# Kernel tuning notes

Hardware: AMD Instinct MI355X
Metric: run time of the kernel (lower is better)

The kernel has to match this reference:

```python
import jax, jax.numpy as jnp
import numpy as np

N = 100_000   # nodes
E = 1_600_000 # edges
F = 128       # feature_dim
H = 128       # hidden_dim
C = 16        # num_classes


def setup_inputs() -> dict:
    key = jax.random.key(0)
    ks = jax.random.split(key, 7)
    x = jax.random.normal(ks[0], (N, F), dtype=jnp.float32)
    edge_index = jax.random.randint(ks[1], (2, E), 0, N, dtype=jnp.int64)
    edge_attr = jax.random.uniform(ks[2], (E,), dtype=jnp.float32)
    W1 = jax.random.normal(ks[3], (F, H), dtype=jnp.float32) / np.float32(np.sqrt(F))
    b1 = jnp.zeros((H,), jnp.float32)
    W2 = jax.random.normal(ks[4], (H, C), dtype=jnp.float32) / np.float32(np.sqrt(H))
    b2 = jnp.zeros((C,), jnp.float32)
    return {"x": x, "edge_index": edge_index, "edge_attr": edge_attr,
            "W1": W1, "b1": b1, "W2": W2, "b2": b2}


def gcn_conv(x, src, dst, ew, W, b, n):
    # PyG GCNConv: add self-loops (weight 1), symmetric degree normalization,
    # linear transform, weighted scatter-sum to destinations, bias after aggregation.
    loop = jnp.arange(n, dtype=src.dtype)
    s = jnp.concatenate([src, loop])
    d = jnp.concatenate([dst, loop])
    w = jnp.concatenate([ew, jnp.ones((n,), ew.dtype)])
    deg = jax.ops.segment_sum(w, d, num_segments=n)           # [N]
    dinv = jnp.where(deg > 0, jax.lax.rsqrt(deg), 0.0)
    norm = dinv[s] * w * dinv[d]                               # [E+N]
    h = x @ W                                                  # [N, out]
    out = jax.ops.segment_sum(h[s] * norm[:, None], d, num_segments=n)
    return out + b


def reference(x, edge_index, edge_attr, W1, b1, W2, b2):
    src, dst = edge_index[0], edge_index[1]
    h = gcn_conv(x, src, dst, edge_attr, W1, b1, N)
    h = jax.nn.relu(h)
    # dropout is identity in eval mode
    h = gcn_conv(h, src, dst, edge_attr, W2, b2, N)
    return jax.nn.softmax(h, axis=1)
```

## Files before the change

### kernel.cpp

```cpp
#include <hip/hip_runtime.h>
#include <hip/hip_fp16.h>
#include <math.h>

#define SCAN_CHUNK 2048
#define NBLK 256
#define BSH 9
#define BNODES 512


typedef __attribute__((ext_vector_type(8))) _Float16 f16x8;
typedef __attribute__((ext_vector_type(16))) float f32x16;


__global__ __launch_bounds__(256) void k_prep(const float* __restrict__ W,
                                              __half* __restrict__ W1f) {
    int tid = blockIdx.x * 256 + threadIdx.x;
    if (tid < 16384) {
        int j  = tid & 7;
        int l  = (tid >> 3) & 63;
        int ks = (tid >> 9) & 7;
        int cb = tid >> 12;
        int c = cb * 32 + (l & 31);
        int k = (l >> 5) * 8 + ks * 16 + j;
        W1f[tid] = __float2half(W[(size_t)k * 128 + c]);
    }
}


__device__ __forceinline__ void gemm1_mfma(const float* __restrict__ x,
                                           const __half* __restrict__ W1f,
                                           __half* __restrict__ h1, int n,
                                           int row0, int t, char* smem) {
    __half (*xs)[136] = (__half (*)[136])smem;
#pragma unroll
    for (int it = 0; it < 4; ++it) {
        int idx = it * 256 + t;
        int r = idx >> 5, c4 = (idx & 31) * 4;
        int gr = row0 + r;
        float4 v = (gr < n) ? *(const float4*)(x + (size_t)gr * 128 + c4)
                            : make_float4(0.f, 0.f, 0.f, 0.f);
        union { __half2 h[2]; uint2 u; } pk;
        pk.h[0] = __floats2half2_rn(v.x, v.y);
        pk.h[1] = __floats2half2_rn(v.z, v.w);
        *(uint2*)&xs[r][c4] = pk.u;
    }
    __syncthreads();

    int wv = t >> 6, lane = t & 63;
    int m = lane & 31, kh = lane >> 5;
    int col0 = wv * 32;

    f16x8 a[8], b[8];
    const __half* bp = W1f + ((size_t)wv * 8 * 64 + lane) * 8;
#pragma unroll
    for (int ks = 0; ks < 8; ++ks)
        b[ks] = *(const f16x8*)(bp + (size_t)ks * 64 * 8);
#pragma unroll
    for (int ks = 0; ks < 8; ++ks)
        a[ks] = *(const f16x8*)&xs[m][kh * 8 + ks * 16];

    f32x16 acc;
#pragma unroll
    for (int r = 0; r < 16; ++r) acc[r] = 0.f;
#pragma unroll
    for (int ks = 0; ks < 8; ++ks)
        acc = __builtin_amdgcn_mfma_f32_32x32x16_f16(a[ks], b[ks], acc, 0, 0, 0);

#pragma unroll
    for (int r = 0; r < 16; ++r) {
        int row = (r & 3) + 8 * (r >> 2) + 4 * kh;
        int g = row0 + row;
        if (g < n) h1[(size_t)g * 128 + col0 + m] = __float2half(acc[r]);
    }
}

__device__ __forceinline__ long long sl_begin(int eb, int e) {
    return ((long long)eb * e / NBLK) & ~3LL;
}


__global__ __launch_bounds__(256) void kA(const int* __restrict__ dst, int e,
                                          int* __restrict__ hist, int nbuck,
                                          const float* __restrict__ x,
                                          const __half* __restrict__ W1f,
                                          __half* __restrict__ h1, int n,
                                          int nbB, int nbG, int gbase) {
    __shared__ char smem[32 * 136 * 2];
    int bid = blockIdx.x;
    long long T = nbB + nbG;
    long long g = ((long long)bid * nbG) / T;
    bool is_g = (((long long)(bid + 1) * nbG) / T) > g;
    int t = threadIdx.x;

    if (!is_g) {
        int* cnt = (int*)smem;
        int eb = bid - (int)g;
        for (int j = t; j < nbuck; j += 256) cnt[j] = 0;
        __syncthreads();
        long long e0 = sl_begin(eb, e);
        long long e1 = (eb == NBLK - 1) ? e : sl_begin(eb + 1, e);
        for (long long i = e0 + (long long)t * 4; i + 3 < e1; i += 1024) {
            int4 d4 = *(const int4*)(dst + i);
            atomicAdd(&cnt[d4.x >> BSH], 1);
            atomicAdd(&cnt[d4.y >> BSH], 1);
            atomicAdd(&cnt[d4.z >> BSH], 1);
            atomicAdd(&cnt[d4.w >> BSH], 1);
        }
        long long vend = e0 + ((e1 - e0) & ~3LL);
        for (long long i = vend + t; i < e1; i += 256)
            atomicAdd(&cnt[dst[i] >> BSH], 1);
        __syncthreads();
        for (int j = t; j < nbuck; j += 256)
            hist[(size_t)j * NBLK + eb] = cnt[j];
        return;
    }

    gemm1_mfma(x, W1f, h1, n, (gbase + (int)g) * 32, t, smem);
}


__global__ __launch_bounds__(256) void k_scanh(int* __restrict__ hist,
                                               int* __restrict__ bsum, int nh) {
    __shared__ int sh[256];
    int b = blockIdx.x, t = threadIdx.x;
    int base = b * SCAN_CHUNK + t * 8;
    int v[8];
    int s = 0;
#pragma unroll
    for (int j = 0; j < 8; ++j) {
        int i = base + j;
        v[j] = (i < nh) ? hist[i] : 0;
        s += v[j];
    }
    sh[t] = s;
    __syncthreads();
    for (int off = 1; off < 256; off <<= 1) {
        int u = (t >= off) ? sh[t - off] : 0;
        __syncthreads();
        sh[t] += u;
        __syncthreads();
    }
    int excl = (t > 0) ? sh[t - 1] : 0;
    if (t == 255) bsum[b] = sh[255];
    int run = excl;
#pragma unroll
    for (int j = 0; j < 8; ++j) {
        int i = base + j;
        if (i < nh) hist[i] = run;
        run += v[j];
    }
}

__device__ __forceinline__ void scan_bsum(const int* __restrict__ bsum, int nbS,
                                          int* boffs, int t) {
    if (t < 32) {
        int raw = (t < nbS) ? bsum[t] : 0;
        int v = raw;
        for (int off = 1; off < 32; off <<= 1) {
            int u = __shfl_up(v, off, 64);
            if (t >= off) v += u;
        }
        boffs[t] = v - raw;
    }
}


__global__ __launch_bounds__(256) void kB(const int* __restrict__ src,
                                          const int* __restrict__ dst,
                                          const float* __restrict__ ew, int e,
                                          const int* __restrict__ hist,
                                          const int* __restrict__ bsum, int nbS,
                                          int nbuck,
                                          int2* __restrict__ bucketed,
                                          const float* __restrict__ x,
                                          const __half* __restrict__ W1f,
                                          __half* __restrict__ h1, int n,
                                          int nbB, int nbG, int gbase) {
    __shared__ char smem[32 * 136 * 2];
    int bid = blockIdx.x;
    long long T = nbB + nbG;
    long long g = ((long long)bid * nbG) / T;
    bool is_g = (((long long)(bid + 1) * nbG) / T) > g;
    int t = threadIdx.x;

    if (!is_g) {
        int* wc = (int*)smem;
        int* boffs = (int*)(smem + 2048);
        int eb = bid - (int)g;
        scan_bsum(bsum, nbS, boffs, t);
        __syncthreads();
        for (int j = t; j < nbuck; j += 256) {
            int idx = j * NBLK + eb;
            wc[j] = hist[idx] + boffs[idx >> 11];
        }
        __syncthreads();
        long long e0 = sl_begin(eb, e);
        long long e1 = (eb == NBLK - 1) ? e : sl_begin(eb + 1, e);
        for (long long i = e0 + (long long)t * 4; i + 3 < e1; i += 1024) {
            int4 d4 = *(const int4*)(dst + i);
            int4 s4 = *(const int4*)(src + i);
            float4 w4 = *(const float4*)(ew + i);
            int2 rec;
            int pos;
            pos = atomicAdd(&wc[d4.x >> BSH], 1);
            rec.x = s4.x | ((d4.x & (BNODES - 1)) << 17);
            rec.y = __float_as_int(w4.x);
            bucketed[pos] = rec;
            pos = atomicAdd(&wc[d4.y >> BSH], 1);
            rec.x = s4.y | ((d4.y & (BNODES - 1)) << 17);
            rec.y = __float_as_int(w4.y);
            bucketed[pos] = rec;
            pos = atomicAdd(&wc[d4.z >> BSH], 1);
            rec.x = s4.z | ((d4.z & (BNODES - 1)) << 17);
            rec.y = __float_as_int(w4.z);
            bucketed[pos] = rec;
            pos = atomicAdd(&wc[d4.w >> BSH], 1);
            rec.x = s4.w | ((d4.w & (BNODES - 1)) << 17);
            rec.y = __float_as_int(w4.w);
            bucketed[pos] = rec;
        }
        long long vend = e0 + ((e1 - e0) & ~3LL);
        for (long long i = vend + t; i < e1; i += 256) {
            int d = dst[i];
            int b = d >> BSH;
            int pos = atomicAdd(&wc[b], 1);
            int2 rec;
            rec.x = src[i] | ((d & (BNODES - 1)) << 17);
            rec.y = __float_as_int(ew[i]);
            bucketed[pos] = rec;
        }
        return;
    }

    gemm1_mfma(x, W1f, h1, n, (gbase + (int)g) * 32, t, smem);
}


__global__ __launch_bounds__(256) void kC(const int2* __restrict__ bucketed,
                                          const int* __restrict__ hist,
                                          const int* __restrict__ bsum, int nbS,
                                          int nbuck, int n, int e,
                                          int2* __restrict__ csr,
                                          int2* __restrict__ nodeinfo,
                                          const float* __restrict__ x,
                                          const __half* __restrict__ W1f,
                                          __half* __restrict__ h1, int gbase) {
    __shared__ char smem[32 * 136 * 2];
    int bid = blockIdx.x, t = threadIdx.x;

    if (bid >= nbuck) {
        gemm1_mfma(x, W1f, h1, n, (gbase + bid - nbuck) * 32, t, smem);
        return;
    }

    int*   cnts  = (int*)smem;
    float* degs  = (float*)(smem + 2048);
    int*   wcs   = (int*)(smem + 4096);
    int*   sh    = (int*)(smem + 6144);
    int*   boffs = (int*)(smem + 7168);
    int b = bid;

    scan_bsum(bsum, nbS, boffs, t);
    cnts[t] = 0; cnts[t + 256] = 0;
    degs[t] = 0.f; degs[t + 256] = 0.f;
    __syncthreads();

    int i0 = b * NBLK;
    int bstart = hist[i0] + boffs[i0 >> 11];
    int bend;
    if (b == nbuck - 1) bend = e;
    else {
        int i1 = (b + 1) * NBLK;
        bend = hist[i1] + boffs[i1 >> 11];
    }

    for (int i = bstart + t; i < bend; i += 256) {
        int2 rec = bucketed[i];
        int l = (rec.x >> 17) & (BNODES - 1);
        atomicAdd(&cnts[l], 1);
        atomicAdd(&degs[l], __int_as_float(rec.y));
    }
    __syncthreads();

    int c0 = cnts[2 * t], c1 = cnts[2 * t + 1];
    sh[t] = c0 + c1;
    __syncthreads();
    for (int off = 1; off < 256; off <<= 1) {
        int u = (t >= off) ? sh[t - off] : 0;
        __syncthreads();
        sh[t] += u;
        __syncthreads();
    }
    int excl = (t > 0) ? sh[t - 1] : 0;

    int rs0 = bstart + excl;
    int rs1 = rs0 + c0;
    wcs[2 * t] = rs0;
    wcs[2 * t + 1] = rs1;
#pragma unroll
    for (int q = 0; q < 2; ++q) {
        int l = 2 * t + q;
        float dv = 1.0f / sqrtf(1.0f + degs[l]);
        int gnode = b * BNODES + l;
        if (gnode < n) {
            int2 ni;
            ni.x = (q == 0) ? rs0 : rs1;
            ni.y = __float_as_int(dv);
            nodeinfo[gnode] = ni;
        }
    }
    if (b == nbuck - 1 && t == 0) {
        int2 sent; sent.x = e; sent.y = 0;
        nodeinfo[n] = sent;
    }
    __syncthreads();

    for (int i = bstart + t; i < bend; i += 256) {
        int2 rec = bucketed[i];
        int l = (rec.x >> 17) & (BNODES - 1);
        int pos = atomicAdd(&wcs[l], 1);
        int2 o;
        o.x = rec.x & 0x1FFFF;
        o.y = rec.y;
        csr[pos] = o;
    }
}


__global__ __launch_bounds__(256) void k_agg1(const __half* __restrict__ h1,
                                              const int2* __restrict__ nodeinfo,
                                              const int2* __restrict__ csr,
                                              const float* __restrict__ b1,
                                              const float* __restrict__ W2g,
                                              __half* __restrict__ h2, int n) {
    __shared__ float a1s[4][128];
    __shared__ float wt[16][132];
    __shared__ float dnl[4];
    int t = threadIdx.x;
#pragma unroll
    for (int it = 0; it < 8; ++it) {
        int idx = it * 256 + t;
        wt[idx & 15][idx >> 4] = W2g[idx];
    }
    int wv = t >> 6;
    int lane = t & 63;
    int grp = lane >> 4;
    int sl = lane & 15;
    int i = blockIdx.x * 4 + wv;
    const int* nis = (const int*)nodeinfo;
    float acc[8];
#pragma unroll
    for (int k = 0; k < 8; ++k) acc[k] = 0.f;
    float di = 0.f;
    if (i < n) {
        int2 ni = nodeinfo[i];
        int begin = ni.x;
        int end = nis[(size_t)(i + 1) * 2];
        di = __int_as_float(ni.y);
        if (lane == 0) dnl[wv] = di;
        if (grp == 0) {
            uint4 sv = *((const uint4*)(h1 + (size_t)i * 128) + sl);
            const __half2* hp = (const __half2*)&sv;
#pragma unroll
            for (int k = 0; k < 4; ++k) {
                float2 f = __half22float2(hp[k]);
                acc[2 * k] = di * f.x; acc[2 * k + 1] = di * f.y;
            }
        }
        int len = end - begin;
        int m = (len + 3) >> 2;
        if (m > 0) {
            int j0 = begin + grp;
            bool v0 = j0 < end;
            int2 er0 = csr[v0 ? j0 : begin];
            float w0 = v0 ? __int_as_float(er0.y) *
                            __int_as_float(nis[2 * (size_t)er0.x + 1]) : 0.f;
            uint4 hv0 = *((const uint4*)(h1 + (size_t)er0.x * 128) + sl);
            int j1 = j0 + 4;
            bool v1 = j1 < end;
            int2 er1 = csr[v1 ? j1 : begin];
            float w1 = v1 ? __int_as_float(er1.y) *
                            __int_as_float(nis[2 * (size_t)er1.x + 1]) : 0.f;
            for (int it2 = 1; it2 < m; ++it2) {
                uint4 hv1 = *((const uint4*)(h1 + (size_t)er1.x * 128) + sl);
                int j2 = j1 + 4;
                bool v2 = j2 < end;
                int2 er2 = csr[v2 ? j2 : begin];
                float w2 = v2 ? __int_as_float(er2.y) *
                                __int_as_float(nis[2 * (size_t)er2.x + 1]) : 0.f;
                const __half2* hp = (const __half2*)&hv0;
#pragma unroll
                for (int k = 0; k < 4; ++k) {
                    float2 f = __half22float2(hp[k]);
                    acc[2 * k]     += w0 * f.x;
                    acc[2 * k + 1] += w0 * f.y;
                }
                hv0 = hv1; w0 = w1;
                er1 = er2; w1 = w2; j1 = j2;
            }
            const __half2* hp = (const __half2*)&hv0;
#pragma unroll
            for (int k = 0; k < 4; ++k) {
                float2 f = __half22float2(hp[k]);
                acc[2 * k]     += w0 * f.x;
                acc[2 * k + 1] += w0 * f.y;
            }
        }
    }
#pragma unroll
    for (int k = 0; k < 8; ++k) {
        acc[k] += __shfl_xor(acc[k], 16, 64);
        acc[k] += __shfl_xor(acc[k], 32, 64);
    }
    if (i < n && grp == 0) {
#pragma unroll
        for (int k = 0; k < 8; ++k)
            a1s[wv][8 * sl + k] = fmaxf(di * acc[k] + b1[8 * sl + k], 0.f);
    }
    __syncthreads();
    int oi = t >> 2, q = t & 3;
    int node = oi >> 4, c = oi & 15;
    const float* arow = a1s[node];
    float accd = 0.f;
#pragma unroll
    for (int j = 0; j < 32; ++j) accd += arow[q + 4 * j] * wt[c][q + 4 * j];
    accd += __shfl_xor(accd, 1, 64);
    accd += __shfl_xor(accd, 2, 64);
    int gi = blockIdx.x * 4 + node;
    if (q == 0 && gi < n) h2[(size_t)gi * 16 + c] = __float2half(dnl[node] * accd);
}


__global__ __launch_bounds__(256) void k_agg2(const __half* __restrict__ h2,
                                              const int2* __restrict__ nodeinfo,
                                              const int2* __restrict__ csr,
                                              const float* __restrict__ b2,
                                              float* __restrict__ out, int n) {
    int t = blockIdx.x * 256 + threadIdx.x;
    int i = t >> 4;
    int c = t & 15;
    if (i >= n) return;
    int2 ni = nodeinfo[i];
    int begin = ni.x;
    int end = ((const int*)nodeinfo)[(size_t)(i + 1) * 2];
    float di = __int_as_float(ni.y);
    float acc = __half2float(h2[(size_t)i * 16 + c]);
    int j = begin;
    for (; j + 4 <= end; j += 4) {
        int2 e0 = csr[j], e1 = csr[j + 1], e2 = csr[j + 2], e3 = csr[j + 3];
        float f0 = __half2float(h2[(size_t)e0.x * 16 + c]);
        float f1 = __half2float(h2[(size_t)e1.x * 16 + c]);
        float f2 = __half2float(h2[(size_t)e2.x * 16 + c]);
        float f3 = __half2float(h2[(size_t)e3.x * 16 + c]);
        acc += __int_as_float(e0.y) * f0;
        acc += __int_as_float(e1.y) * f1;
        acc += __int_as_float(e2.y) * f2;
        acc += __int_as_float(e3.y) * f3;
    }
    for (; j < end; ++j) {
        int2 e0 = csr[j];
        acc += __int_as_float(e0.y) * __half2float(h2[(size_t)e0.x * 16 + c]);
    }
    acc = di * acc + b2[c];
    float m = acc;
    for (int off = 8; off; off >>= 1) m = fmaxf(m, __shfl_xor(m, off, 16));
    float ex = expf(acc - m);
    float ssum = ex;
    for (int off = 8; off; off >>= 1) ssum += __shfl_xor(ssum, off, 16);
    out[(size_t)i * 16 + c] = ex / ssum;
}


extern "C" void kernel_launch(void* const* d_in, const int* in_sizes, int n_in,
                              void* d_out, int out_size, void* d_ws, size_t ws_size,
                              hipStream_t stream) {
    const float* x  = (const float*)d_in[0];
    const int*   ei = (const int*)d_in[1];
    const float* ew = (const float*)d_in[2];
    const float* W1 = (const float*)d_in[3];
    const float* b1 = (const float*)d_in[4];
    const float* W2 = (const float*)d_in[5];
    const float* b2 = (const float*)d_in[6];
    float* out = (float*)d_out;

    const int N = in_sizes[0] / 128;
    const int E = in_sizes[2];
    const int* src = ei;
    const int* dst = ei + E;

    const int nbuck = (N + BNODES - 1) >> BSH;
    const int nh = nbuck * NBLK;
    const int nbS = (nh + SCAN_CHUNK - 1) / SCAN_CHUNK;

    char* w = (char*)d_ws;
    int2*   bucketed = (int2*)w;              w += (size_t)E * 8;
    int2*   csr      = (int2*)w;              w += (size_t)E * 8;
    __half* h1       = (__half*)w;            w += (size_t)N * 128 * 2;
    __half* h2       = (__half*)w;            w += (size_t)N * 16 * 2;
    int2*   nodeinfo = (int2*)w;              w += (size_t)(N + 2) * 8;
    int*    hist     = (int*)w;               w += (size_t)nh * 4;
    int*    bsum     = (int*)w;               w += 64 * 4;
    __half* W1f      = (__half*)w;            w += (size_t)16384 * 2;

    int nbG_total = (N + 31) / 32;
    int nbG3 = 625;
    int nbG1 = (nbG_total - nbG3) / 2;
    int nbG2 = nbG_total - nbG3 - nbG1;

    k_prep<<<64, 256, 0, stream>>>(W1, W1f);
    kA<<<NBLK + nbG1, 256, 0, stream>>>(dst, E, hist, nbuck, x, W1f, h1, N,
                                        NBLK, nbG1, 0);
    k_scanh<<<nbS, 256, 0, stream>>>(hist, bsum, nh);
    kB<<<NBLK + nbG2, 256, 0, stream>>>(src, dst, ew, E, hist, bsum, nbS, nbuck,
                                        bucketed, x, W1f, h1, N, NBLK, nbG2, nbG1);
    kC<<<nbuck + nbG3, 256, 0, stream>>>(bucketed, hist, bsum, nbS, nbuck, N, E,
                                         csr, nodeinfo, x, W1f, h1, nbG1 + nbG2);
    k_agg1<<<(N + 3) / 4, 256, 0, stream>>>(h1, nodeinfo, csr, b1, W2, h2, N);
    k_agg2<<<(N + 15) / 16, 256, 0, stream>>>(h2, nodeinfo, csr, b2, out, N);
}
```

Baseline: 196.7 us.

## Fold source degree normalization into CSR edge weights via split CSR build

Splits the CSR build kernel into two launches. The first computes per-node offsets and inverse-sqrt degrees. The second scatters edges and stores each edge weight already multiplied by dinv[src]. This removes the per-edge random gather of the source's dinv from the layer-1 aggregation. It also stops pre-scaling h2 by dinv, so layer 2 applies dinv to the self term instead. The GEMM work that overlaps with these kernels is redistributed over four launches. The cost is an extra launch and a second pass over the bucketed edges, with the dinv gather moved into the CSR build rather than removed.

```diff
diff --git a/kernel.cpp b/kernel.cpp
--- a/kernel.cpp
+++ b/kernel.cpp
@@ -236,15 +236,14 @@
 }
 
 
-__global__ __launch_bounds__(256) void kC(const int2* __restrict__ bucketed,
-                                          const int* __restrict__ hist,
-                                          const int* __restrict__ bsum, int nbS,
-                                          int nbuck, int n, int e,
-                                          int2* __restrict__ csr,
-                                          int2* __restrict__ nodeinfo,
-                                          const float* __restrict__ x,
-                                          const __half* __restrict__ W1f,
-                                          __half* __restrict__ h1, int gbase) {
+__global__ __launch_bounds__(256) void kC1(const int2* __restrict__ bucketed,
+                                           const int* __restrict__ hist,
+                                           const int* __restrict__ bsum, int nbS,
+                                           int nbuck, int n, int e,
+                                           int2* __restrict__ nodeinfo,
+                                           const float* __restrict__ x,
+                                           const __half* __restrict__ W1f,
+                                           __half* __restrict__ h1, int gbase) {
     __shared__ char smem[32 * 136 * 2];
     int bid = blockIdx.x, t = threadIdx.x;
 
@@ -255,9 +254,8 @@
 
     int*   cnts  = (int*)smem;
     float* degs  = (float*)(smem + 2048);
-    int*   wcs   = (int*)(smem + 4096);
-    int*   sh    = (int*)(smem + 6144);
-    int*   boffs = (int*)(smem + 7168);
+    int*   sh    = (int*)(smem + 4096);
+    int*   boffs = (int*)(smem + 5120);
     int b = bid;
 
     scan_bsum(bsum, nbS, boffs, t);
@@ -295,8 +293,6 @@
 
     int rs0 = bstart + excl;
     int rs1 = rs0 + c0;
-    wcs[2 * t] = rs0;
-    wcs[2 * t + 1] = rs1;
 #pragma unroll
     for (int q = 0; q < 2; ++q) {
         int l = 2 * t + q;
@@ -313,15 +309,58 @@
         int2 sent; sent.x = e; sent.y = 0;
         nodeinfo[n] = sent;
     }
-    __syncthreads();
+}
+
+
+__global__ __launch_bounds__(256) void kC2(const int2* __restrict__ bucketed,
+                                           const int* __restrict__ hist,
+                                           const int* __restrict__ bsum, int nbS,
+                                           int nbuck, int n, int e,
+                                           int2* __restrict__ csr,
+                                           const int2* __restrict__ nodeinfo,
+                                           const float* __restrict__ x,
+                                           const __half* __restrict__ W1f,
+                                           __half* __restrict__ h1, int gbase) {
+    __shared__ char smem[32 * 136 * 2];
+    int bid = blockIdx.x, t = threadIdx.x;
+
+    if (bid >= nbuck) {
+        gemm1_mfma(x, W1f, h1, n, (gbase + bid - nbuck) * 32, t, smem);
+        return;
+    }
+
+    int* wcs   = (int*)smem;
+    int* boffs = (int*)(smem + 2048);
+    int b = bid;
+    const int* nis = (const int*)nodeinfo;
+
+    scan_bsum(bsum, nbS, boffs, t);
+#pragma unroll
+    for (int q = 0; q < 2; ++q) {
+        int l = t + q * 256;
+        int gnode = b * BNODES + l;
+        wcs[l] = (gnode < n) ? nis[2 * (size_t)gnode] : 0;
+    }
+    __syncthreads();
+
+    int i0 = b * NBLK;
+    int bstart = hist[i0] + boffs[i0 >> 11];
+    int bend;
+    if (b == nbuck - 1) bend = e;
+    else {
+        int i1 = (b + 1) * NBLK;
+        bend = hist[i1] + boffs[i1 >> 11];
+    }
 
     for (int i = bstart + t; i < bend; i += 256) {
         int2 rec = bucketed[i];
         int l = (rec.x >> 17) & (BNODES - 1);
+        int s = rec.x & 0x1FFFF;
+        float dv = __int_as_float(nis[2 * (size_t)s + 1]);
         int pos = atomicAdd(&wcs[l], 1);
         int2 o;
-        o.x = rec.x & 0x1FFFF;
-        o.y = rec.y;
+        o.x = s;
+        o.y = __float_as_int(__int_as_float(rec.y) * dv);
         csr[pos] = o;
     }
 }
@@ -335,7 +374,6 @@
                                               __half* __restrict__ h2, int n) {
     __shared__ float a1s[4][128];
     __shared__ float wt[16][132];
-    __shared__ float dnl[4];
     int t = threadIdx.x;
 #pragma unroll
     for (int it = 0; it < 8; ++it) {
@@ -347,7 +385,6 @@
     int grp = lane >> 4;
     int sl = lane & 15;
     int i = blockIdx.x * 4 + wv;
-    const int* nis = (const int*)nodeinfo;
     float acc[8];
 #pragma unroll
     for (int k = 0; k < 8; ++k) acc[k] = 0.f;
@@ -355,9 +392,8 @@
     if (i < n) {
         int2 ni = nodeinfo[i];
         int begin = ni.x;
-        int end = nis[(size_t)(i + 1) * 2];
+        int end = ((const int*)nodeinfo)[(size_t)(i + 1) * 2];
         di = __int_as_float(ni.y);
-        if (lane == 0) dnl[wv] = di;
         if (grp == 0) {
             uint4 sv = *((const uint4*)(h1 + (size_t)i * 128) + sl);
             const __half2* hp = (const __half2*)&sv;
@@ -373,21 +409,18 @@
             int j0 = begin + grp;
             bool v0 = j0 < end;
             int2 er0 = csr[v0 ? j0 : begin];
-            float w0 = v0 ? __int_as_float(er0.y) *
-                            __int_as_float(nis[2 * (size_t)er0.x + 1]) : 0.f;
+            float w0 = v0 ? __int_as_float(er0.y) : 0.f;
             uint4 hv0 = *((const uint4*)(h1 + (size_t)er0.x * 128) + sl);
             int j1 = j0 + 4;
             bool v1 = j1 < end;
             int2 er1 = csr[v1 ? j1 : begin];
-            float w1 = v1 ? __int_as_float(er1.y) *
-                            __int_as_float(nis[2 * (size_t)er1.x + 1]) : 0.f;
+            float w1 = v1 ? __int_as_float(er1.y) : 0.f;
             for (int it2 = 1; it2 < m; ++it2) {
                 uint4 hv1 = *((const uint4*)(h1 + (size_t)er1.x * 128) + sl);
                 int j2 = j1 + 4;
                 bool v2 = j2 < end;
                 int2 er2 = csr[v2 ? j2 : begin];
-                float w2 = v2 ? __int_as_float(er2.y) *
-                                __int_as_float(nis[2 * (size_t)er2.x + 1]) : 0.f;
+                float w2 = v2 ? __int_as_float(er2.y) : 0.f;
                 const __half2* hp = (const __half2*)&hv0;
 #pragma unroll
                 for (int k = 0; k < 4; ++k) {
@@ -427,7 +460,7 @@
     accd += __shfl_xor(accd, 1, 64);
     accd += __shfl_xor(accd, 2, 64);
     int gi = blockIdx.x * 4 + node;
-    if (q == 0 && gi < n) h2[(size_t)gi * 16 + c] = __float2half(dnl[node] * accd);
+    if (q == 0 && gi < n) h2[(size_t)gi * 16 + c] = __float2half(accd);
 }
 
 
@@ -444,7 +477,7 @@
     int begin = ni.x;
     int end = ((const int*)nodeinfo)[(size_t)(i + 1) * 2];
     float di = __int_as_float(ni.y);
-    float acc = __half2float(h2[(size_t)i * 16 + c]);
+    float acc = di * __half2float(h2[(size_t)i * 16 + c]);
     int j = begin;
     for (; j + 4 <= end; j += 4) {
         int2 e0 = csr[j], e1 = csr[j + 1], e2 = csr[j + 2], e3 = csr[j + 3];
@@ -503,9 +536,10 @@
     __half* W1f      = (__half*)w;            w += (size_t)16384 * 2;
 
     int nbG_total = (N + 31) / 32;
-    int nbG3 = 625;
-    int nbG1 = (nbG_total - nbG3) / 2;
-    int nbG2 = nbG_total - nbG3 - nbG1;
+    int nbG1 = 1250;
+    int nbG2 = 1250;
+    int nbG3 = 313;
+    int nbG4 = nbG_total - nbG1 - nbG2 - nbG3;
 
     k_prep<<<64, 256, 0, stream>>>(W1, W1f);
     kA<<<NBLK + nbG1, 256, 0, stream>>>(dst, E, hist, nbuck, x, W1f, h1, N,
@@ -513,8 +547,11 @@
     k_scanh<<<nbS, 256, 0, stream>>>(hist, bsum, nh);
     kB<<<NBLK + nbG2, 256, 0, stream>>>(src, dst, ew, E, hist, bsum, nbS, nbuck,
                                         bucketed, x, W1f, h1, N, NBLK, nbG2, nbG1);
-    kC<<<nbuck + nbG3, 256, 0, stream>>>(bucketed, hist, bsum, nbS, nbuck, N, E,
-                                         csr, nodeinfo, x, W1f, h1, nbG1 + nbG2);
+    kC1<<<nbuck + nbG3, 256, 0, stream>>>(bucketed, hist, bsum, nbS, nbuck, N, E,
+                                          nodeinfo, x, W1f, h1, nbG1 + nbG2);
+    kC2<<<nbuck + nbG4, 256, 0, stream>>>(bucketed, hist, bsum, nbS, nbuck, N, E,
+                                          csr, nodeinfo, x, W1f, h1,
+                                          nbG1 + nbG2 + nbG3);
     k_agg1<<<(N + 3) / 4, 256, 0, stream>>>(h1, nodeinfo, csr, b1, W2, h2, N);
     k_agg2<<<(N + 15) / 16, 256, 0, stream>>>(h2, nodeinfo, csr, b2, out, N);
 }
```

After: 188.4 us. -4.2%, faster.
